# Kernel tuning notes

Hardware: AMD Instinct MI355X
Metric: run time of the kernel (lower is better)

## Reference

```python
import jax, jax.numpy as jnp
import numpy as np

NUM_HEADS = 16
KEY_SIZE = 64
MODEL = NUM_HEADS * KEY_SIZE
B, S = 4, 2048
NEG = jnp.float32(-1e9)


def alibi_bidirectional_bias(num_heads, seq_len):
    # slopes for num_heads//2 heads: 1 / x**(i+1), x = 24**(1/h)
    h = num_heads // 2
    x = 24.0 ** (1.0 / h)
    slopes = (1.0 / x ** jnp.arange(1, h + 1, dtype=jnp.float32))[:, None, None]  # [h,1,1]
    i = jnp.arange(seq_len)
    rel = (i[None, :] - i[:, None]).astype(jnp.float32)  # rel[i,j] = j - i
    # forward (causal): tril(j - i) + (-1e9 strictly above diag)
    fwd = slopes * jnp.tril(rel) + jnp.triu(jnp.full((seq_len, seq_len), NEG), k=1)
    # backward (anti-causal): triu(i - j) + (-1e9 strictly below diag)
    bwd = slopes * jnp.triu(-rel) + jnp.tril(jnp.full((seq_len, seq_len), NEG), k=-1)
    return jnp.concatenate([fwd, bwd], axis=0)  # [num_heads, S, S]


def setup_inputs() -> dict:
    key = jax.random.key(0)
    ks = jax.random.split(key, 11)
    sc = 0.02
    d = {
        "query": jax.random.normal(ks[0], (B, S, MODEL), jnp.float32),
        "key": jax.random.normal(ks[1], (B, S, MODEL), jnp.float32),
        "value": jax.random.normal(ks[2], (B, S, MODEL), jnp.float32),
        "Wq": jax.random.normal(ks[3], (MODEL, MODEL), jnp.float32) * sc,
        "bq": jnp.zeros((MODEL,), jnp.float32),
        "Wk": jax.random.normal(ks[4], (MODEL, MODEL), jnp.float32) * sc,
        "bk": jnp.zeros((MODEL,), jnp.float32),
        "Wv": jax.random.normal(ks[5], (MODEL, MODEL), jnp.float32) * sc,
        "bv": jnp.zeros((MODEL,), jnp.float32),
        "Wo": jax.random.normal(ks[6], (MODEL, MODEL), jnp.float32) * sc,
        "bo": jnp.zeros((MODEL,), jnp.float32),
    }
    return d


def reference(query, key, value, Wq, bq, Wk, bk, Wv, bv, Wo, bo):
    b, s, _ = query.shape
    H, D = NUM_HEADS, KEY_SIZE

    def proj(x, W, bias):
        return (x @ W.T + bias).reshape(b, s, H, D).transpose(0, 2, 1, 3)  # [B,H,S,D]

    q = proj(query, Wq, bq)
    k = proj(key, Wk, bk)
    v = proj(value, Wv, bv)

    bias = alibi_bidirectional_bias(H, s)  # [H,S,S], broadcasts over batch
    scores = jnp.einsum("bhqd,bhkd->bhqk", q, k) / jnp.sqrt(jnp.float32(D)) + bias
    attn = jax.nn.softmax(scores, axis=-1)
    out = jnp.einsum("bhqk,bhkd->bhqd", attn, v)
    out = out.transpose(0, 2, 1, 3).reshape(b, s, H * D)
    return out @ Wo.T + bo
```

## Files before the change

### kernel.cpp

```cpp
#include <hip/hip_runtime.h>
#include <hip/hip_bf16.h>
#include <stdint.h>

typedef unsigned short u16;
typedef __attribute__((ext_vector_type(8))) __bf16 bf16x8;
typedef __attribute__((ext_vector_type(4))) __bf16 bf16x4;
typedef __attribute__((ext_vector_type(4))) float f32x4;

#define S_LEN 2048
#define NHEAD 16
#define HDIM 64
#define DMODEL 1024
#define NBATCH 4
#define MTOK (NBATCH * S_LEN)

__device__ __forceinline__ u16 f2bf(float f) {
    uint32_t u = __float_as_uint(f);
    u += 0x7fffu + ((u >> 16) & 1u);
    return (u16)(u >> 16);
}

__device__ __forceinline__ void gld_lds16(const u16* g, u16* l) {
    __builtin_amdgcn_global_load_lds(
        (const __attribute__((address_space(1))) void*)g,
        (__attribute__((address_space(3))) void*)l, 16, 0, 0);
}

__global__ __launch_bounds__(256) void cast_all(
        const float* __restrict__ q, const float* __restrict__ k, const float* __restrict__ v,
        const float* __restrict__ wq, const float* __restrict__ wk,
        const float* __restrict__ wv, const float* __restrict__ wo,
        u16* __restrict__ xq, u16* __restrict__ xk, u16* __restrict__ xv,
        u16* __restrict__ wqb, u16* __restrict__ wkb, u16* __restrict__ wvb,
        u16* __restrict__ wob) {
    size_t idx4 = (size_t)blockIdx.x * 256 + threadIdx.x;
    const float* src;
    u16* dst;
    size_t off;
    if (idx4 < (size_t)3 << 21) {
        int t = (int)(idx4 >> 21);
        off = (idx4 & ((1u << 21) - 1)) * 4;
        src = (t == 0) ? q : (t == 1) ? k : v;
        dst = (t == 0) ? xq : (t == 1) ? xk : xv;
    } else {
        size_t w = idx4 - ((size_t)3 << 21);
        int t = (int)(w >> 18);
        off = (w & ((1u << 18) - 1)) * 4;
        src = (t == 0) ? wq : (t == 1) ? wk : (t == 2) ? wv : wo;
        dst = (t == 0) ? wqb : (t == 1) ? wkb : (t == 2) ? wvb : wob;
    }
    float4 val = *(const float4*)(src + off);
    ushort4 o;
    o.x = f2bf(val.x); o.y = f2bf(val.y); o.z = f2bf(val.z); o.w = f2bf(val.w);
    *(ushort4*)(dst + off) = o;
}

#define TM 128
#define TN 128
#define BK 64
#define KT (DMODEL / BK)

__device__ __forceinline__ void gemm_body(const u16* __restrict__ A,
                                          const u16* __restrict__ W,
                                          const float* __restrict__ bias,
                                          void* __restrict__ outp, int mode,
                                          int m0, int n0) {
    __shared__ __align__(16) u16 As[3][TM * BK];
    __shared__ __align__(16) u16 Bs[3][TN * BK];
    const int tid  = threadIdx.x;
    const int lane = tid & 63;
    const int wv   = tid >> 6;
    const int l16  = lane & 15;
    const int quad = lane >> 4;
    const int wm   = (wv >> 2) * 64;
    const int wn   = (wv & 3) * 32;

    f32x4 acc[4][2];
#pragma unroll
    for (int i = 0; i < 4; i++)
#pragma unroll
        for (int j = 0; j < 2; j++) acc[i][j] = {};

    const int sr  = lane >> 3;
    const int sc7 = (lane & 7) ^ sr;
    const u16* gA = A + (size_t)(m0 + wv * 16 + sr) * DMODEL + sc7 * 8;
    const u16* gB = W + (size_t)(n0 + wv * 16 + sr) * DMODEL + sc7 * 8;
    const int lofs = wv * 16 * BK;

    const int cA = quad ^ (l16 & 7);
    const int cB = (quad + 4) ^ (l16 & 7);

#define STG(b, t) do { \
    gld_lds16(gA + (size_t)(t) * BK,                    &As[b][lofs]); \
    gld_lds16(gA + (size_t)(t) * BK + 8 * DMODEL,       &As[b][lofs + 8 * BK]); \
    gld_lds16(gB + (size_t)(t) * BK,                    &Bs[b][lofs]); \
    gld_lds16(gB + (size_t)(t) * BK + 8 * DMODEL,       &Bs[b][lofs + 8 * BK]); \
} while (0)

    STG(0, 0);
    STG(1, 1);
    __builtin_amdgcn_s_waitcnt(0x0F74);
    __builtin_amdgcn_sched_barrier(0);
    __builtin_amdgcn_s_barrier();
    __builtin_amdgcn_sched_barrier(0);

    int bc = 0;
#pragma unroll 1
    for (int t = 0; t < KT; ++t) {
        if (t + 2 < KT) {
            int bs = bc + 2; if (bs >= 3) bs -= 3;
            STG(bs, t + 2);
        }
        __builtin_amdgcn_sched_barrier(0);

        bf16x8 af0[4], af1[4], bf0[2], bf1[2];
#pragma unroll
        for (int i = 0; i < 4; i++) {
            const u16* ap = &As[bc][(wm + i * 16 + l16) * BK];
            af0[i] = *(const bf16x8*)(ap + cA * 8);
            af1[i] = *(const bf16x8*)(ap + cB * 8);
        }
#pragma unroll
        for (int j = 0; j < 2; j++) {
            const u16* bp = &Bs[bc][(wn + j * 16 + l16) * BK];
            bf0[j] = *(const bf16x8*)(bp + cA * 8);
            bf1[j] = *(const bf16x8*)(bp + cB * 8);
        }
#pragma unroll
        for (int i = 0; i < 4; i++)
#pragma unroll
            for (int j = 0; j < 2; j++)
                acc[i][j] = __builtin_amdgcn_mfma_f32_16x16x32_bf16(af0[i], bf0[j], acc[i][j], 0, 0, 0);
#pragma unroll
        for (int i = 0; i < 4; i++)
#pragma unroll
            for (int j = 0; j < 2; j++)
                acc[i][j] = __builtin_amdgcn_mfma_f32_16x16x32_bf16(af1[i], bf1[j], acc[i][j], 0, 0, 0);

        if (t + 2 < KT) {
            __builtin_amdgcn_s_waitcnt(0x0F74);
        } else if (t + 1 < KT) {
            __builtin_amdgcn_s_waitcnt(0x0F70);
        }
        __builtin_amdgcn_sched_barrier(0);
        __builtin_amdgcn_s_barrier();
        __builtin_amdgcn_sched_barrier(0);
        if (++bc == 3) bc = 0;
    }
#undef STG

#pragma unroll
    for (int j = 0; j < 2; j++) {
        int n = n0 + wn + j * 16 + l16;
        float bv = bias[n];
#pragma unroll
        for (int i = 0; i < 4; i++) {
            int mbase = m0 + wm + i * 16 + quad * 4;
#pragma unroll
            for (int r = 0; r < 4; r++) {
                int m = mbase + r;
                float v = acc[i][j][r] + bv;
                if (mode == 2) {
                    ((float*)outp)[(size_t)m * DMODEL + n] = v;
                } else {
                    int b = m >> 11, s = m & (S_LEN - 1);
                    int h = n >> 6, d = n & 63;
                    u16* o = (u16*)outp;
                    size_t idx = (mode == 0)
                        ? ((((size_t)(b * NHEAD + h)) * S_LEN + s) * HDIM + d)
                        : ((((size_t)(b * NHEAD + h)) * HDIM + d) * S_LEN + s);
                    o[idx] = f2bf(v);
                }
            }
        }
    }
}

__device__ __forceinline__ void gemm_coords(int& m0, int& n0) {
    const int lid = blockIdx.x + 8 * blockIdx.y;
    const int xcd = lid & 7;
    const int s   = lid >> 3;
    n0 = (s & 7) * TN;
    m0 = ((s >> 3) + 8 * xcd) * TM;
}

__global__ __launch_bounds__(512, 2) void gemm_qkv(
        const u16* __restrict__ xq, const u16* __restrict__ xk, const u16* __restrict__ xv,
        const u16* __restrict__ wq, const u16* __restrict__ wk, const u16* __restrict__ wv,
        const float* __restrict__ bq, const float* __restrict__ bk, const float* __restrict__ bv,
        u16* __restrict__ Qb, u16* __restrict__ Kb, u16* __restrict__ Vb) {
    int z = blockIdx.z;
    const u16* A   = (z == 0) ? xq : (z == 1) ? xk : xv;
    const u16* W   = (z == 0) ? wq : (z == 1) ? wk : wv;
    const float* b = (z == 0) ? bq : (z == 1) ? bk : bv;
    u16* out       = (z == 0) ? Qb : (z == 1) ? Kb : Vb;
    int m0, n0;
    gemm_coords(m0, n0);
    gemm_body(A, W, b, out, (z == 2) ? 1 : 0, m0, n0);
}

__global__ __launch_bounds__(512, 2) void gemm_one(
        const u16* __restrict__ A, const u16* __restrict__ W,
        const float* __restrict__ bias, void* __restrict__ out, int mode) {
    int m0, n0;
    gemm_coords(m0, n0);
    gemm_body(A, W, bias, out, mode, m0, n0);
}

__global__ __launch_bounds__(256, 4) void flash_kernel(
        const u16* __restrict__ Q, const u16* __restrict__ K,
        const u16* __restrict__ Vt, u16* __restrict__ AO) {
    __shared__ __align__(16) u16 Ksm[2][64 * 64];
    __shared__ __align__(16) u16 Vsm[2][64 * 64];
    __shared__ __align__(16) u16 Psm[4][16 * 64];

    const int tid  = threadIdx.x;
    const int wv   = tid >> 6;
    const int lane = tid & 63;
    const int l16  = lane & 15;
    const int quad = lane >> 4;

    const int lid   = blockIdx.x + 16 * blockIdx.y;
    const int xcd   = lid & 7;
    const int slot  = lid >> 3;
    const int bh    = xcd + 8 * (slot >> 4);
    const int g_idx = slot & 15;

    const int h    = bh & (NHEAD - 1);
    const int b    = bh >> 4;
    const bool fwd = (h < 8);
    const int sgn  = fwd ? 1 : -1;
    const float slope2 = __builtin_amdgcn_exp2f(-(float)((h & 7) + 1) * 0.5731203125901445f)
                         * 1.4426950408889634f;
    const float cL = 0.18033688011112042f;

    const u16* Kg = K + (size_t)bh * S_LEN * HDIM;
    const u16* Vg = Vt + (size_t)bh * HDIM * S_LEN;

    const int sr = lane >> 3;
    const int sc = (lane & 7) ^ sr;
    const int r0 = 16 * wv;

    const int cA = quad ^ (l16 & 7);
    const int cB = (quad + 4) ^ (l16 & 7);

    float brt[4][4];
#pragma unroll
    for (int t = 0; t < 4; t++)
#pragma unroll
        for (int r = 0; r < 4; r++)
            brt[t][r] = slope2 * (float)(sgn * (16 * t + 4 * quad + r - l16)) - 16.0f;

    int poff4[4];
#pragma unroll
    for (int t = 0; t < 4; t++)
        poff4[t] = l16 * 64 + (((2 * t + (quad >> 1)) ^ (l16 & 7)) * 8) + 4 * (quad & 1);

    bf16x8 ones;
#pragma unroll
    for (int j = 0; j < 8; j++) ones[j] = (__bf16)1.0f;

    const float dkq = slope2 * (float)(sgn * 64);

#pragma unroll 1
    for (int half = 0; half < 2; half++) {
        const int g  = half ? (31 - g_idx) : g_idx;
        const int q0 = g * 64 + wv * 16;
        const u16* Qp = Q + ((size_t)bh * S_LEN + q0) * HDIM;
        const bf16x8 aq0 = *(const bf16x8*)(Qp + l16 * HDIM + quad * 8);
        const bf16x8 aq1 = *(const bf16x8*)(Qp + l16 * HDIM + 32 + quad * 8);

        f32x4 o[4], osum = {};
#pragma unroll
        for (int dt = 0; dt < 4; dt++) o[dt] = {};

        const int kt0 = fwd ? 0 : g;
        const int kt1 = fwd ? g : (S_LEN / 64 - 1);

        __syncthreads();
        const u16* kg = Kg + ((size_t)(kt0 * 64) + r0 + sr) * 64 + sc * 8;
        const u16* vg = Vg + (size_t)(r0 + sr) * S_LEN + kt0 * 64 + sc * 8;
        gld_lds16(kg,              &Ksm[0][r0 * 64]);
        gld_lds16(kg + 8 * 64,     &Ksm[0][(r0 + 8) * 64]);
        gld_lds16(vg,              &Vsm[0][r0 * 64]);
        gld_lds16(vg + 8 * S_LEN,  &Vsm[0][(r0 + 8) * 64]);
        kg += 64 * 64;
        vg += 64;

        float kq = slope2 * (float)(sgn * (kt0 * 64 - q0));

        int buf = 0;
        for (int kt = kt0; kt <= kt1; ++kt) {
            __builtin_amdgcn_s_waitcnt(0x0F70);
            __syncthreads();
            if (kt < kt1) {
                gld_lds16(kg,             &Ksm[buf ^ 1][r0 * 64]);
                gld_lds16(kg + 8 * 64,    &Ksm[buf ^ 1][(r0 + 8) * 64]);
                gld_lds16(vg,             &Vsm[buf ^ 1][r0 * 64]);
                gld_lds16(vg + 8 * S_LEN, &Vsm[buf ^ 1][(r0 + 8) * 64]);
                kg += 64 * 64;
                vg += 64;
            }
            const u16* Ks = &Ksm[buf][0];
            const u16* Vs = &Vsm[buf][0];

            f32x4 st[4];
            __builtin_amdgcn_s_setprio(1);
#pragma unroll
            for (int t = 0; t < 4; t++) {
                const u16* kp = Ks + (16 * t + l16) * 64;
                bf16x8 k0 = *(const bf16x8*)(kp + cA * 8);
                bf16x8 k1 = *(const bf16x8*)(kp + cB * 8);
                f32x4 c = {};
                c = __builtin_amdgcn_mfma_f32_16x16x32_bf16(k0, aq0, c, 0, 0, 0);
                c = __builtin_amdgcn_mfma_f32_16x16x32_bf16(k1, aq1, c, 0, 0, 0);
                st[t] = c;
            }
            __builtin_amdgcn_s_setprio(0);

            float p[4][4];
            if (kt == g) {
                const int qg = q0 + l16;
#pragma unroll
                for (int t = 0; t < 4; t++)
#pragma unroll
                    for (int r = 0; r < 4; r++) {
                        const int kg2 = kt * 64 + 16 * t + 4 * quad + r;
                        const bool ok = fwd ? (kg2 <= qg) : (kg2 >= qg);
                        float s2 = fmaf(st[t][r], cL, brt[t][r] + kq);
                        p[t][r] = ok ? __builtin_amdgcn_exp2f(s2) : 0.0f;
                    }
            } else {
#pragma unroll
                for (int t = 0; t < 4; t++)
#pragma unroll
                    for (int r = 0; r < 4; r++)
                        p[t][r] = __builtin_amdgcn_exp2f(fmaf(st[t][r], cL, brt[t][r] + kq));
            }
            kq += dkq;

            u16* Pw = &Psm[wv][0];
#pragma unroll
            for (int t = 0; t < 4; t++) {
                bf16x4 pk;
                pk[0] = (__bf16)p[t][0];
                pk[1] = (__bf16)p[t][1];
                pk[2] = (__bf16)p[t][2];
                pk[3] = (__bf16)p[t][3];
                *(bf16x4*)(Pw + poff4[t]) = pk;
            }
            __builtin_amdgcn_s_waitcnt(0xC07F);
            bf16x8 pf0 = *(const bf16x8*)(&Pw[l16 * 64 + cA * 8]);
            bf16x8 pf1 = *(const bf16x8*)(&Pw[l16 * 64 + cB * 8]);

            __builtin_amdgcn_s_setprio(1);
#pragma unroll
            for (int dt = 0; dt < 4; dt++) {
                const u16* vp = Vs + (dt * 16 + l16) * 64;
                bf16x8 v0 = *(const bf16x8*)(vp + cA * 8);
                bf16x8 v1 = *(const bf16x8*)(vp + cB * 8);
                o[dt] = __builtin_amdgcn_mfma_f32_16x16x32_bf16(pf0, v0, o[dt], 0, 0, 0);
                o[dt] = __builtin_amdgcn_mfma_f32_16x16x32_bf16(pf1, v1, o[dt], 0, 0, 0);
            }
            osum = __builtin_amdgcn_mfma_f32_16x16x32_bf16(pf0, ones, osum, 0, 0, 0);
            osum = __builtin_amdgcn_mfma_f32_16x16x32_bf16(pf1, ones, osum, 0, 0, 0);
            __builtin_amdgcn_s_setprio(0);
            buf ^= 1;
        }

#pragma unroll
        for (int r = 0; r < 4; r++) {
            float inv = 1.0f / osum[r];
            int qg = q0 + quad * 4 + r;
            u16* op = AO + ((size_t)b * S_LEN + qg) * DMODEL + h * HDIM;
#pragma unroll
            for (int dt = 0; dt < 4; dt++)
                op[dt * 16 + l16] = f2bf(o[dt][r] * inv);
        }
    }
}

extern "C" void kernel_launch(void* const* d_in, const int* in_sizes, int n_in,
                              void* d_out, int out_size, void* d_ws, size_t ws_size,
                              hipStream_t stream) {
    const float* query = (const float*)d_in[0];
    const float* key   = (const float*)d_in[1];
    const float* value = (const float*)d_in[2];
    const float* Wq    = (const float*)d_in[3];
    const float* bq    = (const float*)d_in[4];
    const float* Wk    = (const float*)d_in[5];
    const float* bk    = (const float*)d_in[6];
    const float* Wv    = (const float*)d_in[7];
    const float* bv    = (const float*)d_in[8];
    const float* Wo    = (const float*)d_in[9];
    const float* bo    = (const float*)d_in[10];

    const size_t Xe = (size_t)MTOK * DMODEL;
    const size_t We = (size_t)DMODEL * DMODEL;
    u16* xq  = (u16*)d_ws;
    u16* xk  = xq + Xe;
    u16* xv  = xk + Xe;
    u16* wqb = xv + Xe;
    u16* wkb = wqb + We;
    u16* wvb = wkb + We;
    u16* wob = wvb + We;
    u16* Qb  = wob + We;
    u16* Kb  = Qb + Xe;
    u16* Vb  = Kb + Xe;
    u16* AO  = xq;

    cast_all<<<dim3(28672), dim3(256), 0, stream>>>(
        query, key, value, Wq, Wk, Wv, Wo,
        xq, xk, xv, wqb, wkb, wvb, wob);

    gemm_qkv<<<dim3(DMODEL / TN, MTOK / TM, 3), dim3(512), 0, stream>>>(
        xq, xk, xv, wqb, wkb, wvb, bq, bk, bv, Qb, Kb, Vb);

    flash_kernel<<<dim3(16, NBATCH * NHEAD), dim3(256), 0, stream>>>(Qb, Kb, Vb, AO);

    gemm_one<<<dim3(DMODEL / TN, MTOK / TM), dim3(512), 0, stream>>>(AO, wob, bo, d_out, 2);
}
```

Before: 363.0 us.

## Restructure GEMM to 4 waves with 64x64 warp tiles and BK=32

```diff
diff --git a/kernel.cpp b/kernel.cpp
--- a/kernel.cpp
+++ b/kernel.cpp
@@ -57,8 +57,8 @@
 
 #define TM 128
 #define TN 128
-#define BK 64
-#define KT (DMODEL / BK)
+#define BK 32
+#define NKT (DMODEL / BK)
 
 __device__ __forceinline__ void gemm_body(const u16* __restrict__ A,
                                           const u16* __restrict__ W,
@@ -66,35 +66,34 @@
                                           void* __restrict__ outp, int mode,
                                           int m0, int n0) {
     __shared__ __align__(16) u16 As[3][TM * BK];
-    __shared__ __align__(16) u16 Bs[3][TN * BK];
+    __shared__ __align__(16) u16 Bs[3][TM * BK];
     const int tid  = threadIdx.x;
     const int lane = tid & 63;
     const int wv   = tid >> 6;
     const int l16  = lane & 15;
     const int quad = lane >> 4;
-    const int wm   = (wv >> 2) * 64;
-    const int wn   = (wv & 3) * 32;
-
-    f32x4 acc[4][2];
+    const int wm   = (wv >> 1) * 64;
+    const int wn   = (wv & 1) * 64;
+
+    f32x4 acc[4][4];
 #pragma unroll
     for (int i = 0; i < 4; i++)
 #pragma unroll
-        for (int j = 0; j < 2; j++) acc[i][j] = {};
-
-    const int sr  = lane >> 3;
-    const int sc7 = (lane & 7) ^ sr;
-    const u16* gA = A + (size_t)(m0 + wv * 16 + sr) * DMODEL + sc7 * 8;
-    const u16* gB = W + (size_t)(n0 + wv * 16 + sr) * DMODEL + sc7 * 8;
-    const int lofs = wv * 16 * BK;
-
-    const int cA = quad ^ (l16 & 7);
-    const int cB = (quad + 4) ^ (l16 & 7);
+        for (int j = 0; j < 4; j++) acc[i][j] = {};
+
+    const int sr  = lane >> 2;
+    const int sc3 = (lane & 3) ^ ((lane >> 3) & 3);
+    const u16* gA = A + (size_t)(m0 + wv * 32 + sr) * DMODEL + sc3 * 8;
+    const u16* gB = W + (size_t)(n0 + wv * 32 + sr) * DMODEL + sc3 * 8;
+    const int lofs = wv * 32 * BK;
+
+    const int cA = quad ^ ((l16 >> 1) & 3);
 
 #define STG(b, t) do { \
-    gld_lds16(gA + (size_t)(t) * BK,                    &As[b][lofs]); \
-    gld_lds16(gA + (size_t)(t) * BK + 8 * DMODEL,       &As[b][lofs + 8 * BK]); \
-    gld_lds16(gB + (size_t)(t) * BK,                    &Bs[b][lofs]); \
-    gld_lds16(gB + (size_t)(t) * BK + 8 * DMODEL,       &Bs[b][lofs + 8 * BK]); \
+    gld_lds16(gA + (size_t)(t) * BK,                      &As[b][lofs]); \
+    gld_lds16(gA + (size_t)(t) * BK + (size_t)16 * DMODEL, &As[b][lofs + 16 * BK]); \
+    gld_lds16(gB + (size_t)(t) * BK,                      &Bs[b][lofs]); \
+    gld_lds16(gB + (size_t)(t) * BK + (size_t)16 * DMODEL, &Bs[b][lofs + 16 * BK]); \
 } while (0)
 
     STG(0, 0);
@@ -106,40 +105,31 @@
 
     int bc = 0;
 #pragma unroll 1
-    for (int t = 0; t < KT; ++t) {
-        if (t + 2 < KT) {
+    for (int t = 0; t < NKT; ++t) {
+        if (t + 2 < NKT) {
             int bs = bc + 2; if (bs >= 3) bs -= 3;
             STG(bs, t + 2);
         }
         __builtin_amdgcn_sched_barrier(0);
 
-        bf16x8 af0[4], af1[4], bf0[2], bf1[2];
-#pragma unroll
-        for (int i = 0; i < 4; i++) {
-            const u16* ap = &As[bc][(wm + i * 16 + l16) * BK];
-            af0[i] = *(const bf16x8*)(ap + cA * 8);
-            af1[i] = *(const bf16x8*)(ap + cB * 8);
-        }
-#pragma unroll
-        for (int j = 0; j < 2; j++) {
-            const u16* bp = &Bs[bc][(wn + j * 16 + l16) * BK];
-            bf0[j] = *(const bf16x8*)(bp + cA * 8);
-            bf1[j] = *(const bf16x8*)(bp + cB * 8);
-        }
+        const u16* Ab = &As[bc][0];
+        const u16* Bb = &Bs[bc][0];
+        bf16x8 af[4], bf[4];
 #pragma unroll
         for (int i = 0; i < 4; i++)
-#pragma unroll
-            for (int j = 0; j < 2; j++)
-                acc[i][j] = __builtin_amdgcn_mfma_f32_16x16x32_bf16(af0[i], bf0[j], acc[i][j], 0, 0, 0);
+            af[i] = *(const bf16x8*)(Ab + (wm + i * 16 + l16) * BK + cA * 8);
+#pragma unroll
+        for (int j = 0; j < 4; j++)
+            bf[j] = *(const bf16x8*)(Bb + (wn + j * 16 + l16) * BK + cA * 8);
 #pragma unroll
         for (int i = 0; i < 4; i++)
 #pragma unroll
-            for (int j = 0; j < 2; j++)
-                acc[i][j] = __builtin_amdgcn_mfma_f32_16x16x32_bf16(af1[i], bf1[j], acc[i][j], 0, 0, 0);
-
-        if (t + 2 < KT) {
+            for (int j = 0; j < 4; j++)
+                acc[i][j] = __builtin_amdgcn_mfma_f32_16x16x32_bf16(af[i], bf[j], acc[i][j], 0, 0, 0);
+
+        if (t + 2 < NKT) {
             __builtin_amdgcn_s_waitcnt(0x0F74);
-        } else if (t + 1 < KT) {
+        } else if (t + 1 < NKT) {
             __builtin_amdgcn_s_waitcnt(0x0F70);
         }
         __builtin_amdgcn_sched_barrier(0);
@@ -150,7 +140,7 @@
 #undef STG
 
 #pragma unroll
-    for (int j = 0; j < 2; j++) {
+    for (int j = 0; j < 4; j++) {
         int n = n0 + wn + j * 16 + l16;
         float bv = bias[n];
 #pragma unroll
@@ -184,7 +174,7 @@
     m0 = ((s >> 3) + 8 * xcd) * TM;
 }
 
-__global__ __launch_bounds__(512, 2) void gemm_qkv(
+__global__ __launch_bounds__(256) void gemm_qkv(
         const u16* __restrict__ xq, const u16* __restrict__ xk, const u16* __restrict__ xv,
         const u16* __restrict__ wq, const u16* __restrict__ wk, const u16* __restrict__ wv,
         const float* __restrict__ bq, const float* __restrict__ bk, const float* __restrict__ bv,
@@ -199,7 +189,7 @@
     gemm_body(A, W, b, out, (z == 2) ? 1 : 0, m0, n0);
 }
 
-__global__ __launch_bounds__(512, 2) void gemm_one(
+__global__ __launch_bounds__(256) void gemm_one(
         const u16* __restrict__ A, const u16* __restrict__ W,
         const float* __restrict__ bias, void* __restrict__ out, int mode) {
     int m0, n0;
@@ -413,10 +403,10 @@
         query, key, value, Wq, Wk, Wv, Wo,
         xq, xk, xv, wqb, wkb, wvb, wob);
 
-    gemm_qkv<<<dim3(DMODEL / TN, MTOK / TM, 3), dim3(512), 0, stream>>>(
+    gemm_qkv<<<dim3(DMODEL / TN, MTOK / TM, 3), dim3(256), 0, stream>>>(
         xq, xk, xv, wqb, wkb, wvb, bq, bk, bv, Qb, Kb, Vb);
 
     flash_kernel<<<dim3(16, NBATCH * NHEAD), dim3(256), 0, stream>>>(Qb, Kb, Vb, AO);
 
-    gemm_one<<<dim3(DMODEL / TN, MTOK / TM), dim3(512), 0, stream>>>(AO, wob, bo, d_out, 2);
-}
+    gemm_one<<<dim3(DMODEL / TN, MTOK / TM), dim3(256), 0, stream>>>(AO, wob, bo, d_out, 2);
+}
```

Result: faster. 329.9 us (-9.1%).
